# Kernel tuning notes

Measured on AMD Instinct MI355X. Metric: run time of the kernel, lower is better.

Reference implementation:

```python
import jax, jax.numpy as jnp
import numpy as np

MIN_NORM = 1e-15
PROJ_EPS = 4e-3  # HGCN float32 boundary eps
C = 1.0          # curvature (all layers)
N_BRANCH = 4


def artanh(x):
    return jnp.arctanh(jnp.clip(x, -1.0 + 1e-7, 1.0 - 1e-7))


def _norm(x):
    return jnp.clip(jnp.linalg.norm(x, axis=-1, keepdims=True), MIN_NORM)


def proj(x, c):
    n = _norm(x)
    maxn = (1.0 - PROJ_EPS) / jnp.sqrt(c)
    return jnp.where(n > maxn, x / n * maxn, x)


def expmap0(u, c):
    sc = jnp.sqrt(c)
    n = _norm(u)
    return jnp.tanh(sc * n) * u / (sc * n)


def logmap0(p, c):
    sc = jnp.sqrt(c)
    n = _norm(p)
    return artanh(sc * n) * p / (sc * n)


def mobius_add(x, y, c):
    x2 = jnp.sum(x * x, -1, keepdims=True)
    y2 = jnp.sum(y * y, -1, keepdims=True)
    xy = jnp.sum(x * y, -1, keepdims=True)
    num = (1.0 + 2.0 * c * xy + c * y2) * x + (1.0 - c * x2) * y
    den = 1.0 + 2.0 * c * xy + c * c * x2 * y2
    return num / jnp.clip(den, MIN_NORM)


def mobius_matvec(W, x, c):
    sc = jnp.sqrt(c)
    xn = _norm(x)
    mx = x @ W.T
    mxn = _norm(mx)
    res = jnp.tanh(mxn / xn * artanh(sc * xn)) * mx / (mxn * sc)
    zero = jnp.all(mx == 0, axis=-1, keepdims=True)
    return jnp.where(zero, jnp.zeros((), x.dtype), res)


def mobius_mulscaler(r, x, c):
    sc = jnp.sqrt(c)
    xn = _norm(x)
    return jnp.tanh(r * artanh(sc * xn)) * x / (xn * sc)


def spmm(src, dst, w, xt, n):
    # out[i] = sum_{e: dst[e]=i} w[e] * xt[src[e]]
    return jax.ops.segment_sum(w[:, None] * xt[src], dst, num_segments=n)


def hgc_layer(h, W, b, src, dst, w, n):
    # HypLinear (dropout=0)
    h = proj(mobius_matvec(W, h, C), C)
    hb = proj(expmap0(b[None, :], C), C)
    h = proj(mobius_add(h, hb, C), C)
    # HypAgg: sparse propagation in tangent space
    st = spmm(src, dst, w, logmap0(h, C), n)
    h = proj(expmap0(st, C), C)
    # HypAct (relu)
    return proj(expmap0(jax.nn.relu(logmap0(h, C)), C), C)


def encode(x, W0, b0, W1, b1, src, dst, w, n):
    h = proj(expmap0(x, C), C)  # proj_tan0 is identity on Poincare ball
    h = hgc_layer(h, W0, b0, src, dst, w, n)
    h = hgc_layer(h, W1, b1, src, dst, w, n)
    return h


def setup_inputs() -> dict:
    key = jax.random.key(0)
    ks = jax.random.split(key, 8)
    N, F_IN, HID, DIM, E = 50000, 128, 128, 64, 1600000
    x = jax.random.normal(ks[0], (N, F_IN), jnp.float32)
    edge_src = jax.random.randint(ks[1], (E,), 0, N, jnp.int32)
    edge_dst = jax.random.randint(ks[2], (E,), 0, N, jnp.int32)
    # positive, roughly row-normalized edge weights (avg degree 32)
    edge_w = jax.random.uniform(ks[3], (N_BRANCH, E), jnp.float32) / 32.0
    W0 = jax.random.normal(ks[4], (N_BRANCH, HID, F_IN), jnp.float32) * 0.05
    b0 = jax.random.normal(ks[5], (N_BRANCH, HID), jnp.float32) * 0.01
    W1 = jax.random.normal(ks[6], (N_BRANCH, DIM, HID), jnp.float32) * 0.05
    b1 = jax.random.normal(ks[7], (N_BRANCH, DIM), jnp.float32) * 0.01
    return {"x": x, "edge_src": edge_src, "edge_dst": edge_dst, "edge_w": edge_w,
            "W0": W0, "b0": b0, "W1": W1, "b1": b1}


def reference(x, edge_src, edge_dst, edge_w, W0, b0, W1, b1):
    n = x.shape[0]
    # 4 directional-proximity branches (d_i, d_o, n_i, n_o); fixed small loop
    branches = [encode(x, W0[i], b0[i], W1[i], b1[i], edge_src, edge_dst, edge_w[i], n)
                for i in range(N_BRANCH)]
    # Mobius-weighted (scalar 1/8) combination, left-to-right mobius_add chain
    target = mobius_mulscaler(0.125, branches[0], C)
    for br in branches[1:]:
        target = mobius_add(target, mobius_mulscaler(0.125, br, C), C)
    feat = jnp.stack(branches + [target], axis=1)  # [N, 5, dim]
    # HypAttnAgg (use_att=False) with row-normalized per-node star adjacency:
    # target row of each 5-block = mean of the 5 tangent vectors
    agg = logmap0(feat, C).mean(axis=1)            # [N, dim]
    return proj(expmap0(agg, C), C)
```

## Files before the change

kernel.cpp:

```cpp
#include <hip/hip_runtime.h>
#include <math.h>

#define MAXN_P 0.996f

typedef unsigned short bfraw;
typedef __attribute__((ext_vector_type(8))) short bf16x8;
typedef __attribute__((ext_vector_type(4))) float f32x4;

__device__ __forceinline__ float wred(float v){
  #pragma unroll
  for(int o=32;o>0;o>>=1) v += __shfl_xor(v,o,64);
  return v;
}
template<int W>
__device__ __forceinline__ float gredw(float v){
  #pragma unroll
  for(int o=W/2;o>0;o>>=1) v += __shfl_xor(v,o,64);
  return v;
}
__device__ __forceinline__ float artanh_c(float x){
  x = fminf(fmaxf(x, -1.0f+1e-7f), 1.0f-1e-7f);
  return atanhf(x);
}
__device__ __forceinline__ float sel4(float4 w, int g){
  float ab = (g&1) ? w.y : w.x;
  float cd = (g&1) ? w.w : w.z;
  return (g&2) ? cd : ab;
}
__device__ __forceinline__ bfraw f2bf(float f){
  unsigned u = __float_as_uint(f);
  unsigned r = (u + 0x7fffu + ((u>>16)&1u)) >> 16;
  return (bfraw)r;
}
__device__ __forceinline__ float bflo(unsigned u){ return __uint_as_float(u<<16); }
__device__ __forceinline__ float bfhi(unsigned u){ return __uint_as_float(u & 0xffff0000u); }

__device__ __forceinline__ void acc8(float* a, float w, uint4 u){
  a[0]=fmaf(w, bflo(u.x), a[0]); a[1]=fmaf(w, bfhi(u.x), a[1]);
  a[2]=fmaf(w, bflo(u.y), a[2]); a[3]=fmaf(w, bfhi(u.y), a[3]);
  a[4]=fmaf(w, bflo(u.z), a[4]); a[5]=fmaf(w, bfhi(u.z), a[5]);
  a[6]=fmaf(w, bflo(u.w), a[6]); a[7]=fmaf(w, bfhi(u.w), a[7]);
}

template<int W, int K>
__device__ __forceinline__ float postK(const float* u, float* h){
  float ss = 0.f;
  #pragma unroll
  for(int k=0;k<K;k++) ss += u[k]*u[k];
  ss = gredw<W>(ss);
  float un = fmaxf(sqrtf(ss), 1e-15f);
  float t1 = tanhf(un);
  float sc = t1/un;
  float pn = t1;
  if (pn > MAXN_P){ sc *= MAXN_P/pn; pn = MAXN_P; }
  float ln = fmaxf(pn, 1e-15f);
  float m = sc * (artanh_c(ln)/ln);
  float v[K]; float vs = 0.f;
  #pragma unroll
  for(int k=0;k<K;k++){ v[k] = fmaxf(u[k]*m, 0.f); vs += v[k]*v[k]; }
  vs = gredw<W>(vs);
  float vn = fmaxf(sqrtf(vs), 1e-15f);
  float t2 = tanhf(vn);
  float qs = t2/vn;
  float qn = t2;
  if (qn > MAXN_P){ qs *= MAXN_P/qn; qn = MAXN_P; }
  #pragma unroll
  for(int k=0;k<K;k++) h[k] = v[k]*qs;
  return qn;
}

__global__ __launch_bounds__(256) void k_prologue(
    const float* __restrict__ x, bfraw* __restrict__ h0, float* __restrict__ n0, int N,
    const int* __restrict__ dst, int* __restrict__ cnt, int E,
    const float* __restrict__ W0, bfraw* __restrict__ w0b, int nW0,
    const float* __restrict__ W1, bfraw* __restrict__ w1b, int nW1,
    const float* __restrict__ b0, const float* __restrict__ b1,
    float* __restrict__ hb0, float* __restrict__ hb1, int HID, int DIM,
    int RB, int HIST, int W0B, int W1B)
{
  int b = blockIdx.x;
  int tid = threadIdx.x;
  if (b < RB){
    int wid = (b*256 + tid)>>6;
    int lane = tid & 63;
    if (wid >= N) return;
    const float* r = x + (size_t)wid*128;
    float u0 = r[lane], u1 = r[lane+64];
    float ss = wred(u0*u0 + u1*u1);
    float un = fmaxf(sqrtf(ss), 1e-15f);
    float tn = tanhf(un);
    float sc = tn/un;
    float pn = tn;
    if (pn > MAXN_P){ sc *= MAXN_P/pn; pn = MAXN_P; }
    h0[(size_t)wid*128 + lane]      = f2bf(u0*sc);
    h0[(size_t)wid*128 + lane + 64] = f2bf(u1*sc);
    if (lane == 0) n0[wid] = pn;
    return;
  }
  b -= RB;
  if (b < HIST){
    int e = b*256 + tid;
    if (e < E) atomicAdd(&cnt[dst[e]], 1);
    return;
  }
  b -= HIST;
  if (b < W0B){
    int i = b*256 + tid;
    if (i < nW0) w0b[i] = f2bf(W0[i]);
    return;
  }
  b -= W0B;
  if (b < W1B){
    int i = b*256 + tid;
    if (i < nW1) w1b[i] = f2bf(W1[i]);
    return;
  }
  b -= W1B;
  {
    if (tid >= 64) return;
    int layer = b >> 2, br = b & 3;
    int D = layer ? DIM : HID;
    const float* bb = layer ? (b1 + (size_t)br*DIM) : (b0 + (size_t)br*HID);
    float* o        = layer ? (hb1 + (size_t)br*DIM) : (hb0 + (size_t)br*HID);
    float v0 = (tid < D) ? bb[tid] : 0.f;
    float v1 = (tid+64 < D) ? bb[tid+64] : 0.f;
    float ss = wred(v0*v0 + v1*v1);
    float n = fmaxf(sqrtf(ss), 1e-15f);
    float tn = tanhf(n);
    float sc = tn/n;
    if (tn > MAXN_P) sc *= MAXN_P/tn;
    if (tid < D)    o[tid]    = v0*sc;
    if (tid+64 < D) o[tid+64] = v1*sc;
  }
}

__global__ __launch_bounds__(256) void k_scan1(const int* __restrict__ cnt, int* __restrict__ bsum, int N){
  __shared__ int sh[256];
  int base = blockIdx.x*2048;
  int tid = threadIdx.x;
  int loc = 0;
  #pragma unroll
  for(int j=0;j<8;j++){
    int i = base + tid*8 + j;
    loc += (i < N) ? cnt[i] : 0;
  }
  sh[tid] = loc;
  __syncthreads();
  for(int off=128; off>0; off>>=1){
    if (tid < off) sh[tid] += sh[tid+off];
    __syncthreads();
  }
  if (tid == 0) bsum[blockIdx.x] = sh[0];
}
__global__ void k_scan2(int* __restrict__ bsum, int nb){
  if (threadIdx.x == 0){
    int run = 0;
    for(int i=0;i<nb;i++){ int t = bsum[i]; bsum[i] = run; run += t; }
  }
}
__global__ __launch_bounds__(256) void k_scan3(const int* __restrict__ cnt, const int* __restrict__ bsum,
                                               int* __restrict__ rowptr, int* __restrict__ cursor, int N){
  __shared__ int sh[256];
  int base = blockIdx.x*2048;
  int tid = threadIdx.x;
  int v[8]; int loc = 0;
  #pragma unroll
  for(int j=0;j<8;j++){
    int i = base + tid*8 + j;
    v[j] = (i < N) ? cnt[i] : 0;
    loc += v[j];
  }
  sh[tid] = loc;
  __syncthreads();
  for(int off=1; off<256; off<<=1){
    int add = (tid>=off) ? sh[tid-off] : 0;
    __syncthreads();
    sh[tid] += add;
    __syncthreads();
  }
  int run = ((tid==0) ? 0 : sh[tid-1]) + bsum[blockIdx.x];
  #pragma unroll
  for(int j=0;j<8;j++){
    int i = base + tid*8 + j;
    if (i < N){
      rowptr[i] = run; cursor[i] = run; run += v[j];
      if (i == N-1) rowptr[N] = run;
    }
  }
}

__global__ void k_fill(const int* __restrict__ src, const int* __restrict__ dst,
                       const float* __restrict__ ew, int E,
                       int* __restrict__ cursor, int* __restrict__ srcs,
                       float4* __restrict__ wq){
  int e = blockIdx.x*blockDim.x + threadIdx.x;
  if (e >= E) return;
  int d = dst[e];
  int pos = atomicAdd(&cursor[d], 1);
  srcs[pos] = src[e];
  wq[pos] = make_float4(ew[e], ew[(size_t)E + e], ew[2*(size_t)E + e], ew[3*(size_t)E + e]);
}

template<int CT>
__global__ __launch_bounds__(256) void k_gemm_fused(
    const bfraw* __restrict__ Abase, int lda, int abroff,
    const bfraw* __restrict__ Wb,
    const float* __restrict__ nin, int nstride, int nbroff,
    const float* __restrict__ hball,
    bfraw* __restrict__ xt,
    int M)
{
  constexpr int BN = CT*16;
  __shared__ bfraw tile[64*BN];
  int br = blockIdx.z;
  const bfraw* A = Abase + (size_t)br*abroff;
  const bfraw* W = Wb + (size_t)br*BN*128;
  const float* hb = hball + (size_t)br*BN;
  int rb = blockIdx.x*64;
  int t = threadIdx.x;
  int wave = t>>6, lane = t&63;
  int cl = lane&15, grp = lane>>4;

  int rowA = rb + wave*16 + cl;
  bf16x8 afr[4];
  bf16x8 zf = {0,0,0,0,0,0,0,0};
  #pragma unroll
  for(int ks=0;ks<4;ks++){
    if (rowA < M) afr[ks] = *(const bf16x8*)(A + (size_t)rowA*lda + ks*32 + grp*8);
    else          afr[ks] = zf;
  }
  f32x4 acc[CT];
  #pragma unroll
  for(int ct=0;ct<CT;ct++) acc[ct] = f32x4{0.f,0.f,0.f,0.f};
  #pragma unroll
  for(int ct=0;ct<CT;ct++){
    #pragma unroll
    for(int ks=0;ks<4;ks++){
      bf16x8 bfr = *(const bf16x8*)(W + (size_t)(ct*16+cl)*128 + ks*32 + grp*8);
      acc[ct] = __builtin_amdgcn_mfma_f32_16x16x32_bf16(afr[ks], bfr, acc[ct], 0,0,0);
    }
  }
  float hv[CT]; float hb2 = 0.f;
  #pragma unroll
  for(int ct=0;ct<CT;ct++){ hv[ct] = hb[cl+16*ct]; hb2 += hv[ct]*hv[ct]; }
  hb2 = gredw<16>(hb2);
  #pragma unroll
  for(int j=0;j<4;j++){
    int rloc = wave*16 + grp*4 + j;
    int node = rb + rloc;
    bool v = node < M;
    float m[CT]; float ss = 0.f;
    #pragma unroll
    for(int ct=0;ct<CT;ct++){ m[ct] = acc[ct][j]; ss += m[ct]*m[ct]; }
    ss = gredw<16>(ss);
    float mxn_raw = sqrtf(ss);
    float mxn = fmaxf(mxn_raw, 1e-15f);
    float xn = fmaxf(v ? nin[(size_t)node*nstride + br*nbroff] : 1.f, 1e-15f);
    float th = tanhf(mxn/xn * artanh_c(xn));
    float hs = (mxn_raw > 0.f) ? th/mxn : 0.f;
    float hn = (mxn_raw > 0.f) ? th : 0.f;
    if (hn > MAXN_P){ hs *= MAXN_P/hn; hn = MAXN_P; }
    float h[CT]; float xy = 0.f, x2 = 0.f;
    #pragma unroll
    for(int ct=0;ct<CT;ct++){ h[ct] = m[ct]*hs; xy += h[ct]*hv[ct]; x2 += h[ct]*h[ct]; }
    xy = gredw<16>(xy); x2 = gredw<16>(x2);
    float c1 = 1.f + 2.f*xy + hb2;
    float c2 = 1.f - x2;
    float den = fmaxf(1.f + 2.f*xy + x2*hb2, 1e-15f);
    float a[CT]; float as = 0.f;
    #pragma unroll
    for(int ct=0;ct<CT;ct++){ a[ct] = (c1*h[ct] + c2*hv[ct])/den; as += a[ct]*a[ct]; }
    as = gredw<16>(as);
    float an = fmaxf(sqrtf(as), 1e-15f);
    float s2 = 1.f;
    if (an > MAXN_P){ s2 = MAXN_P/an; an = MAXN_P; }
    float ls = artanh_c(an)/an * s2;
    #pragma unroll
    for(int ct=0;ct<CT;ct++) tile[rloc*BN + cl + 16*ct] = f2bf(a[ct]*ls);
  }
  __syncthreads();
  constexpr int IT = (64*BN)/(256*8);
  #pragma unroll
  for(int i=0;i<IT;i++){
    int flat = (t + i*256)*8;
    int row = flat/BN, col = flat%BN;
    int node = rb + row;
    if (node < M)
      *(uint4*)(xt + ((size_t)node*4 + br)*BN + col) = *(const uint4*)(tile + row*BN + col);
  }
}

__global__ __launch_bounds__(256) void k_spmm_l0(const int* __restrict__ rowptr,
                        const int* __restrict__ srcs, const float4* __restrict__ wq,
                        const bfraw* __restrict__ xt,
                        bfraw* __restrict__ hout, float* __restrict__ n4, int N){
  int wid = (blockIdx.x*blockDim.x + threadIdx.x)>>6;
  int lane = threadIdx.x & 63;
  if (wid >= N) return;
  int g = lane>>4;
  float acc[8] = {0,0,0,0,0,0,0,0};
  int p0 = rowptr[wid], p1 = rowptr[wid+1];
  int p = p0;
  for (; p+8 <= p1; p += 8){
    int s[8]; float4 w[8]; uint4 u[8];
    #pragma unroll
    for(int i=0;i<8;i++){ s[i] = srcs[p+i]; w[i] = wq[p+i]; }
    #pragma unroll
    for(int i=0;i<8;i++) u[i] = *((const uint4*)(xt + (size_t)s[i]*512) + lane);
    #pragma unroll
    for(int i=0;i<8;i++) acc8(acc, sel4(w[i],g), u[i]);
  }
  for (; p+2 <= p1; p += 2){
    int s0 = srcs[p], s1 = srcs[p+1];
    float4 w0 = wq[p], w1 = wq[p+1];
    uint4 u0 = *((const uint4*)(xt + (size_t)s0*512) + lane);
    uint4 u1 = *((const uint4*)(xt + (size_t)s1*512) + lane);
    acc8(acc, sel4(w0,g), u0);
    acc8(acc, sel4(w1,g), u1);
  }
  if (p < p1){
    int s0 = srcs[p];
    float4 w0 = wq[p];
    uint4 u0 = *((const uint4*)(xt + (size_t)s0*512) + lane);
    acc8(acc, sel4(w0,g), u0);
  }
  float h[8];
  float qn = postK<16,8>(acc, h);
  uint4 o;
  o.x = (unsigned)f2bf(h[0]) | ((unsigned)f2bf(h[1])<<16);
  o.y = (unsigned)f2bf(h[2]) | ((unsigned)f2bf(h[3])<<16);
  o.z = (unsigned)f2bf(h[4]) | ((unsigned)f2bf(h[5])<<16);
  o.w = (unsigned)f2bf(h[6]) | ((unsigned)f2bf(h[7])<<16);
  *((uint4*)(hout + (size_t)wid*512) + lane) = o;
  if ((lane&15)==0) n4[(size_t)wid*4 + g] = qn;
}

__global__ __launch_bounds__(256) void k_spmm_l1(const int* __restrict__ rowptr,
                        const int* __restrict__ srcs, const float4* __restrict__ wq,
                        const bfraw* __restrict__ xt,
                        float* __restrict__ out, int N){
  int wpair = (blockIdx.x*blockDim.x + threadIdx.x)>>6;
  int lane = threadIdx.x & 63;
  int half = lane>>5;
  int l31 = lane & 31;
  int row = wpair*2 + half;
  bool rv = row < N;
  int rc = rv ? row : 0;
  int p0 = rowptr[rc];
  int p1 = rv ? rowptr[rc+1] : p0;
  int deg = p1 - p0;
  int mx = deg;
  #pragma unroll
  for(int o=32;o>0;o>>=1) mx = max(mx, __shfl_xor(mx, o, 64));
  int g = l31 >> 3;
  int slot = l31 & 7;
  float acc[8] = {0,0,0,0,0,0,0,0};
  for (int i = 0; i < mx; i += 4){
    int pe[4]; float wv[4]; uint4 u[4];
    #pragma unroll
    for(int j=0;j<4;j++){
      int pi = p0 + i + j;
      bool v = pi < p1;
      pe[j] = v ? pi : 0;
      wv[j] = v ? 1.f : 0.f;
    }
    int s[4]; float4 w4[4];
    #pragma unroll
    for(int j=0;j<4;j++){ s[j] = srcs[pe[j]]; w4[j] = wq[pe[j]]; }
    #pragma unroll
    for(int j=0;j<4;j++) u[j] = *((const uint4*)(xt + (size_t)s[j]*256) + l31);
    #pragma unroll
    for(int j=0;j<4;j++) acc8(acc, wv[j]*sel4(w4[j],g), u[j]);
  }
  float h[8];
  float qn = postK<8,8>(acc, h);
  int hb = half*32;
  float t[8], s[8];
  float qk0 = fmaxf(__shfl(qn, hb + 0, 64), 1e-15f);
  float lk0 = artanh_c(qk0)/qk0;
  float s0 = tanhf(0.125f*artanh_c(qk0))/qk0;
  #pragma unroll
  for(int j=0;j<8;j++){
    float xv = __shfl(h[j], hb + slot, 64);
    t[j] = s0*xv;
    s[j] = lk0*xv;
  }
  #pragma unroll
  for(int k=1;k<4;k++){
    float qk = fmaxf(__shfl(qn, hb + k*8, 64), 1e-15f);
    float lk = artanh_c(qk)/qk;
    float sy = tanhf(0.125f*artanh_c(qk))/qk;
    float y[8];
    float dx=0.f, dy=0.f, dxy=0.f;
    #pragma unroll
    for(int j=0;j<8;j++){
      float xv = __shfl(h[j], hb + k*8 + slot, 64);
      y[j] = sy*xv;
      s[j] = fmaf(lk, xv, s[j]);
      dx += t[j]*t[j]; dy += y[j]*y[j]; dxy += t[j]*y[j];
    }
    float x2 = gredw<8>(dx);
    float y2 = gredw<8>(dy);
    float xy = gredw<8>(dxy);
    float c1 = 1.f + 2.f*xy + y2;
    float c2 = 1.f - x2;
    float den = fmaxf(1.f + 2.f*xy + x2*y2, 1e-15f);
    #pragma unroll
    for(int j=0;j<8;j++) t[j] = (c1*t[j] + c2*y[j])/den;
  }
  float dt = 0.f;
  #pragma unroll
  for(int j=0;j<8;j++) dt += t[j]*t[j];
  float tn = fmaxf(sqrtf(gredw<8>(dt)), 1e-15f);
  float lt = artanh_c(tn)/tn;
  #pragma unroll
  for(int j=0;j<8;j++) s[j] = 0.2f*fmaf(lt, t[j], s[j]);
  float ds = 0.f;
  #pragma unroll
  for(int j=0;j<8;j++) ds += s[j]*s[j];
  float an = fmaxf(sqrtf(gredw<8>(ds)), 1e-15f);
  float on = tanhf(an);
  float osc = on/an;
  if (on > MAXN_P) osc *= MAXN_P/on;
  if (g == 0 && rv){
    float* orow = out + (size_t)row*64 + slot*8;
    *(float4*)(orow)     = make_float4(s[0]*osc, s[1]*osc, s[2]*osc, s[3]*osc);
    *(float4*)(orow + 4) = make_float4(s[4]*osc, s[5]*osc, s[6]*osc, s[7]*osc);
  }
}

extern "C" void kernel_launch(void* const* d_in, const int* in_sizes, int n_in,
                              void* d_out, int out_size, void* d_ws, size_t ws_size,
                              hipStream_t stream){
  const float* x   = (const float*)d_in[0];
  const int*   src = (const int*)d_in[1];
  const int*   dst = (const int*)d_in[2];
  const float* ew  = (const float*)d_in[3];
  const float* W0  = (const float*)d_in[4];
  const float* b0  = (const float*)d_in[5];
  const float* W1  = (const float*)d_in[6];
  const float* b1  = (const float*)d_in[7];
  float* out = (float*)d_out;

  const int FIN = 128;
  int N = in_sizes[0]/FIN;
  int E = in_sizes[1];
  int HID = in_sizes[5]/4;
  int DIM = in_sizes[7]/4;

  char* ws = (char*)d_ws;
  size_t off = 0;
  auto alloc = [&](size_t bytes)->char*{
    char* p = ws + off;
    off += (bytes + 255) & ~(size_t)255;
    return p;
  };
  bfraw* h4b    = (bfraw*)alloc((size_t)N*4*FIN*2);
  bfraw* xtb    = (bfraw*)alloc((size_t)N*4*FIN*2);
  float* n0     = (float*)alloc((size_t)N*4);
  float* n4     = (float*)alloc((size_t)N*16);
  int*   rowptr = (int*)alloc((size_t)(N+1)*4);
  int*   cnt    = (int*)alloc((size_t)N*4);
  int*   cursor = (int*)alloc((size_t)N*4);
  int*   srcs   = (int*)alloc((size_t)E*4);
  float4* wq    = (float4*)alloc((size_t)E*16);
  float* hb0    = (float*)alloc((size_t)4*HID*4);
  float* hb1    = (float*)alloc((size_t)4*DIM*4);
  bfraw* w0b    = (bfraw*)alloc((size_t)4*HID*FIN*2);
  bfraw* w1b    = (bfraw*)alloc((size_t)4*DIM*HID*2);
  int*   bsum   = (int*)alloc((size_t)256*4);
  (void)ws_size; (void)n_in; (void)out_size;

  bfraw* h0 = h4b;

  int rowBlocks = (N + 3)/4;
  int pairBlocks = (N + 7)/8;
  int nW0 = 4*HID*FIN, nW1 = 4*DIM*HID;
  int RB = rowBlocks;
  int HIST = (E + 255)/256;
  int W0B = (nW0 + 255)/256;
  int W1B = (nW1 + 255)/256;
  int nscan = (N + 2047)/2048;

  hipMemsetAsync(cnt, 0, (size_t)N*4, stream);
  k_prologue<<<RB + HIST + W0B + W1B + 8, 256, 0, stream>>>(
      x, h0, n0, N, dst, cnt, E, W0, w0b, nW0, W1, w1b, nW1,
      b0, b1, hb0, hb1, HID, DIM, RB, HIST, W0B, W1B);

  k_scan1<<<nscan, 256, 0, stream>>>(cnt, bsum, N);
  k_scan2<<<1, 64, 0, stream>>>(bsum, nscan);
  k_scan3<<<nscan, 256, 0, stream>>>(cnt, bsum, rowptr, cursor, N);
  k_fill<<<HIST, 256, 0, stream>>>(src, dst, ew, E, cursor, srcs, wq);

  k_gemm_fused<8><<<dim3((N+63)/64, 1, 4), 256, 0, stream>>>(
      h0, FIN, 0, w0b, n0, 1, 0, hb0, xtb, N);
  k_spmm_l0<<<rowBlocks, 256, 0, stream>>>(rowptr, srcs, wq, xtb, h4b, n4, N);

  k_gemm_fused<4><<<dim3((N+63)/64, 1, 4), 256, 0, stream>>>(
      h4b, 4*HID, HID, w1b, n4, 4, 1, hb1, xtb, N);
  k_spmm_l1<<<pairBlocks, 256, 0, stream>>>(rowptr, srcs, wq, xtb, out, N);
}
```

Baseline: 677.0 us.

## Merge scan phases and co-schedule CSR fill with layer-0 GEMM

The single-thread block-sum scan kernel is folded into the third scan pass, so each block sums its preceding block totals itself. The CSR fill (atomic cursor scatter) and the layer-0 fused GEMM are independent, so they now run as one launch with block-index dispatch and can overlap on the GPU. This removes two kernel launches and the serial gaps between them. In exchange, each scan block does a serial prefix over up to 25 entries, and the GEMM body is duplicated with CT fixed at 8.

```diff
diff --git a/kernel.cpp b/kernel.cpp
--- a/kernel.cpp
+++ b/kernel.cpp
@@ -152,17 +152,17 @@
   }
   if (tid == 0) bsum[blockIdx.x] = sh[0];
 }
-__global__ void k_scan2(int* __restrict__ bsum, int nb){
-  if (threadIdx.x == 0){
+__global__ __launch_bounds__(256) void k_scan23(const int* __restrict__ cnt, const int* __restrict__ bsum,
+                                                int* __restrict__ rowptr, int* __restrict__ cursor, int N){
+  __shared__ int sh[256];
+  __shared__ int sbase;
+  int tid = threadIdx.x;
+  if (tid == 0){
     int run = 0;
-    for(int i=0;i<nb;i++){ int t = bsum[i]; bsum[i] = run; run += t; }
-  }
-}
-__global__ __launch_bounds__(256) void k_scan3(const int* __restrict__ cnt, const int* __restrict__ bsum,
-                                               int* __restrict__ rowptr, int* __restrict__ cursor, int N){
-  __shared__ int sh[256];
+    for(int i=0;i<(int)blockIdx.x;i++) run += bsum[i];
+    sbase = run;
+  }
   int base = blockIdx.x*2048;
-  int tid = threadIdx.x;
   int v[8]; int loc = 0;
   #pragma unroll
   for(int j=0;j<8;j++){
@@ -178,7 +178,7 @@
     sh[tid] += add;
     __syncthreads();
   }
-  int run = ((tid==0) ? 0 : sh[tid-1]) + bsum[blockIdx.x];
+  int run = ((tid==0) ? 0 : sh[tid-1]) + sbase;
   #pragma unroll
   for(int j=0;j<8;j++){
     int i = base + tid*8 + j;
@@ -189,16 +189,108 @@
   }
 }
 
-__global__ void k_fill(const int* __restrict__ src, const int* __restrict__ dst,
-                       const float* __restrict__ ew, int E,
-                       int* __restrict__ cursor, int* __restrict__ srcs,
-                       float4* __restrict__ wq){
-  int e = blockIdx.x*blockDim.x + threadIdx.x;
-  if (e >= E) return;
-  int d = dst[e];
-  int pos = atomicAdd(&cursor[d], 1);
-  srcs[pos] = src[e];
-  wq[pos] = make_float4(ew[e], ew[(size_t)E + e], ew[2*(size_t)E + e], ew[3*(size_t)E + e]);
+__global__ __launch_bounds__(256) void k_fill_gemm0(
+    const int* __restrict__ src, const int* __restrict__ dst,
+    const float* __restrict__ ew, int E,
+    int* __restrict__ cursor, int* __restrict__ srcs, float4* __restrict__ wq,
+    int FILLB,
+    const bfraw* __restrict__ Abase,
+    const bfraw* __restrict__ Wb,
+    const float* __restrict__ nin,
+    const float* __restrict__ hball,
+    bfraw* __restrict__ xt,
+    int M, int GX)
+{
+  constexpr int CT = 8;
+  constexpr int BN = CT*16;
+  __shared__ bfraw tile[64*BN];
+  int blk = blockIdx.x;
+  int t = threadIdx.x;
+  if (blk < FILLB){
+    int e = blk*256 + t;
+    if (e >= E) return;
+    int d = dst[e];
+    int pos = atomicAdd(&cursor[d], 1);
+    srcs[pos] = src[e];
+    wq[pos] = make_float4(ew[e], ew[(size_t)E + e], ew[2*(size_t)E + e], ew[3*(size_t)E + e]);
+    return;
+  }
+  int bb = blk - FILLB;
+  int br = bb / GX;
+  int rb = (bb - br*GX) * 64;
+  const bfraw* A = Abase;
+  const bfraw* W = Wb + (size_t)br*BN*128;
+  const float* hb = hball + (size_t)br*BN;
+  int wave = t>>6, lane = t&63;
+  int cl = lane&15, grp = lane>>4;
+
+  int rowA = rb + wave*16 + cl;
+  bf16x8 afr[4];
+  bf16x8 zf = {0,0,0,0,0,0,0,0};
+  #pragma unroll
+  for(int ks=0;ks<4;ks++){
+    if (rowA < M) afr[ks] = *(const bf16x8*)(A + (size_t)rowA*128 + ks*32 + grp*8);
+    else          afr[ks] = zf;
+  }
+  f32x4 acc[CT];
+  #pragma unroll
+  for(int ct=0;ct<CT;ct++) acc[ct] = f32x4{0.f,0.f,0.f,0.f};
+  #pragma unroll
+  for(int ct=0;ct<CT;ct++){
+    #pragma unroll
+    for(int ks=0;ks<4;ks++){
+      bf16x8 bfr = *(const bf16x8*)(W + (size_t)(ct*16+cl)*128 + ks*32 + grp*8);
+      acc[ct] = __builtin_amdgcn_mfma_f32_16x16x32_bf16(afr[ks], bfr, acc[ct], 0,0,0);
+    }
+  }
+  float hv[CT]; float hb2 = 0.f;
+  #pragma unroll
+  for(int ct=0;ct<CT;ct++){ hv[ct] = hb[cl+16*ct]; hb2 += hv[ct]*hv[ct]; }
+  hb2 = gredw<16>(hb2);
+  #pragma unroll
+  for(int j=0;j<4;j++){
+    int rloc = wave*16 + grp*4 + j;
+    int node = rb + rloc;
+    bool v = node < M;
+    float m[CT]; float ss = 0.f;
+    #pragma unroll
+    for(int ct=0;ct<CT;ct++){ m[ct] = acc[ct][j]; ss += m[ct]*m[ct]; }
+    ss = gredw<16>(ss);
+    float mxn_raw = sqrtf(ss);
+    float mxn = fmaxf(mxn_raw, 1e-15f);
+    float xn = fmaxf(v ? nin[node] : 1.f, 1e-15f);
+    float th = tanhf(mxn/xn * artanh_c(xn));
+    float hs = (mxn_raw > 0.f) ? th/mxn : 0.f;
+    float hn = (mxn_raw > 0.f) ? th : 0.f;
+    if (hn > MAXN_P){ hs *= MAXN_P/hn; hn = MAXN_P; }
+    float h[CT]; float xy = 0.f, x2 = 0.f;
+    #pragma unroll
+    for(int ct=0;ct<CT;ct++){ h[ct] = m[ct]*hs; xy += h[ct]*hv[ct]; x2 += h[ct]*h[ct]; }
+    xy = gredw<16>(xy); x2 = gredw<16>(x2);
+    float c1 = 1.f + 2.f*xy + hb2;
+    float c2 = 1.f - x2;
+    float den = fmaxf(1.f + 2.f*xy + x2*hb2, 1e-15f);
+    float a[CT]; float as = 0.f;
+    #pragma unroll
+    for(int ct=0;ct<CT;ct++){ a[ct] = (c1*h[ct] + c2*hv[ct])/den; as += a[ct]*a[ct]; }
+    as = gredw<16>(as);
+    float an = fmaxf(sqrtf(as), 1e-15f);
+    float s2 = 1.f;
+    if (an > MAXN_P){ s2 = MAXN_P/an; an = MAXN_P; }
+    float ls = artanh_c(an)/an * s2;
+    #pragma unroll
+    for(int ct=0;ct<CT;ct++) tile[rloc*BN + cl + 16*ct] = f2bf(a[ct]*ls);
+  }
+  __syncthreads();
+  constexpr int IT = (64*BN)/(256*8);
+  #pragma unroll
+  for(int i=0;i<IT;i++){
+    int flat = (t + i*256)*8;
+    int row = flat/BN, col = flat%BN;
+    int node = rb + row;
+    if (node < M)
+      *(uint4*)(xt + ((size_t)node*4 + br)*BN + col) = *(const uint4*)(tile + row*BN + col);
+  }
 }
 
 template<int CT>
@@ -481,6 +573,7 @@
   int W0B = (nW0 + 255)/256;
   int W1B = (nW1 + 255)/256;
   int nscan = (N + 2047)/2048;
+  int GX = (N + 63)/64;
 
   hipMemsetAsync(cnt, 0, (size_t)N*4, stream);
   k_prologue<<<RB + HIST + W0B + W1B + 8, 256, 0, stream>>>(
@@ -488,15 +581,15 @@
       b0, b1, hb0, hb1, HID, DIM, RB, HIST, W0B, W1B);
 
   k_scan1<<<nscan, 256, 0, stream>>>(cnt, bsum, N);
-  k_scan2<<<1, 64, 0, stream>>>(bsum, nscan);
-  k_scan3<<<nscan, 256, 0, stream>>>(cnt, bsum, rowptr, cursor, N);
-  k_fill<<<HIST, 256, 0, stream>>>(src, dst, ew, E, cursor, srcs, wq);
-
-  k_gemm_fused<8><<<dim3((N+63)/64, 1, 4), 256, 0, stream>>>(
-      h0, FIN, 0, w0b, n0, 1, 0, hb0, xtb, N);
+  k_scan23<<<nscan, 256, 0, stream>>>(cnt, bsum, rowptr, cursor, N);
+
+  k_fill_gemm0<<<HIST + GX*4, 256, 0, stream>>>(
+      src, dst, ew, E, cursor, srcs, wq, HIST,
+      h0, w0b, n0, hb0, xtb, N, GX);
+
   k_spmm_l0<<<rowBlocks, 256, 0, stream>>>(rowptr, srcs, wq, xtb, h4b, n4, N);
 
-  k_gemm_fused<4><<<dim3((N+63)/64, 1, 4), 256, 0, stream>>>(
+  k_gemm_fused<4><<<dim3(GX, 1, 4), 256, 0, stream>>>(
       h4b, 4*HID, HID, w1b, n4, 4, 1, hb1, xtb, N);
   k_spmm_l1<<<pairBlocks, 256, 0, stream>>>(rowptr, srcs, wq, xtb, out, N);
 }
```

Measured after the change: 675.2 us. No clear change (-0.3%).
